# Kernel optimization log

Hardware: AMD Instinct MI355X
Metric: run time of the kernel (lower is better)

## Reference

```python
import jax, jax.numpy as jnp
import numpy as np
import math

B, T, D, H = 4, 2048, 1024, 16
DH = D // H

def setup_inputs() -> dict:
    key = jax.random.key(0)
    ks = jax.random.split(key, 5)
    scale = 1.0 / math.sqrt(D)
    x = jax.random.normal(ks[0], (B, T, D), dtype=jnp.float32)
    Wq = jax.random.normal(ks[1], (D, D), dtype=jnp.float32) * scale
    Wk = jax.random.normal(ks[2], (D, D), dtype=jnp.float32) * scale
    Wv = jax.random.normal(ks[3], (D, D), dtype=jnp.float32) * scale
    Wo = jax.random.normal(ks[4], (D, D), dtype=jnp.float32) * scale
    mask = jnp.tril(jnp.ones((T, T), dtype=jnp.int32))  # causal, 1=keep
    return {"x": x, "mask": mask, "Wq": Wq, "Wk": Wk, "Wv": Wv, "Wo": Wo}

def reference(x, mask, Wq, Wk, Wv, Wo):
    Bx, Tx, Dx = x.shape
    # nn.Linear(bias=False): y = x @ W.T
    q = (x @ Wq.T).reshape(Bx, Tx, H, DH).transpose(0, 2, 1, 3)  # [B,H,T,dh]
    k = (x @ Wk.T).reshape(Bx, Tx, H, DH).transpose(0, 2, 1, 3)
    v = (x @ Wv.T).reshape(Bx, Tx, H, DH).transpose(0, 2, 1, 3)
    scores = jnp.einsum('bhqd,bhkd->bhqk', q, k) / math.sqrt(DH)
    m = mask[None, None, :, :]  # [1,1,T,T]
    scores = scores + (m == 0).astype(scores.dtype) * -1e9
    attn = jax.nn.softmax(scores, axis=-1)  # stable (max-subtract) like original
    out = jnp.einsum('bhqk,bhkd->bhqd', attn, v)
    out = out.transpose(0, 2, 1, 3).reshape(Bx, Tx, Dx)
    return out @ Wo.T
```

## Files before the change

### kernel.cpp

```cpp
#include <hip/hip_runtime.h>
#include <stdint.h>

#define B_  4
#define T_  2048
#define D_  1024
#define H_  16
#define DH_ 64

typedef unsigned short u16;
typedef __attribute__((ext_vector_type(8))) short bf16x8;
typedef __attribute__((ext_vector_type(8))) unsigned short u16x8;
typedef __attribute__((ext_vector_type(4))) unsigned short u16x4;
typedef __attribute__((ext_vector_type(4))) float f32x4;

#define NT_ ((size_t)B_ * T_ * D_)
#define QSCALE 0.18033688011112043f

__device__ __forceinline__ u16 f2bf(float f) {
    union { float f; uint32_t u; } v; v.f = f;
    uint32_t r = v.u + 0x7FFFu + ((v.u >> 16) & 1u);
    return (u16)(r >> 16);
}

__device__ __forceinline__ uint32_t pack2(float lo, float hi) {
    union { float f; uint32_t u; } a, b; a.f = lo; b.f = hi;
    return __builtin_amdgcn_perm(b.u, a.u, 0x07060302u);
}

__device__ __forceinline__ void gl2lds16(const u16* g, u16* l) {
    __builtin_amdgcn_global_load_lds(
        (const __attribute__((address_space(1))) unsigned int*)g,
        (__attribute__((address_space(3))) unsigned int*)l,
        16, 0, 0);
}

#define VMCNT(n) asm volatile("s_waitcnt vmcnt(" #n ")" ::: "memory")

__global__ __launch_bounds__(256) void cvt_x_kernel(
    const float* __restrict__ src, u16* __restrict__ dst, int n8)
{
    int i = blockIdx.x * 256 + threadIdx.x;
    if (i >= n8) return;
    f32x4 a = ((const f32x4*)src)[2 * i];
    f32x4 b = ((const f32x4*)src)[2 * i + 1];
    u16x8 o;
    o[0]=f2bf(a[0]); o[1]=f2bf(a[1]); o[2]=f2bf(a[2]); o[3]=f2bf(a[3]);
    o[4]=f2bf(b[0]); o[5]=f2bf(b[1]); o[6]=f2bf(b[2]); o[7]=f2bf(b[3]);
    ((u16x8*)dst)[i] = o;
}

__global__ __launch_bounds__(256) void cvt_w_kernel(
    const float* __restrict__ w0, const float* __restrict__ w1,
    const float* __restrict__ w2, const float* __restrict__ w3,
    u16* __restrict__ dst)
{
    const float* src = (blockIdx.y == 0) ? w0 : (blockIdx.y == 1) ? w1
                     : (blockIdx.y == 2) ? w2 : w3;
    u16* d = dst + (size_t)blockIdx.y * (D_ * D_);
    int i = blockIdx.x * 256 + threadIdx.x;
    f32x4 a = ((const f32x4*)src)[2 * i];
    f32x4 b = ((const f32x4*)src)[2 * i + 1];
    u16x8 o;
    o[0]=f2bf(a[0]); o[1]=f2bf(a[1]); o[2]=f2bf(a[2]); o[3]=f2bf(a[3]);
    o[4]=f2bf(b[0]); o[5]=f2bf(b[1]); o[6]=f2bf(b[2]); o[7]=f2bf(b[3]);
    ((u16x8*)d)[i] = o;
}

template<int OUT_MODE>
__global__ __launch_bounds__(512) void gemm8_kernel(
    const u16* __restrict__ X, const u16* __restrict__ W,
    void* __restrict__ C, int M, int N, int K)
{
    __shared__ __align__(16) u16 Ab2[2][256 * 64];
    __shared__ __align__(16) u16 Bb2[2][256 * 64];

    const int tid  = threadIdx.x;
    const int wave = tid >> 6;
    const int lane = tid & 63;
    const int lq = lane >> 4, lm = lane & 15;
    const int wm = wave >> 2;
    const int wn = wave & 3;

    const int GX  = M >> 8;
    const int nwg = GX * (N >> 8);
    const int cpx = nwg >> 3;
    const int swz = ((int)blockIdx.x & 7) * cpx + ((int)blockIdx.x >> 3);
    const int m0 = (swz % GX) << 8;
    const int n0 = (swz / GX) << 8;

    const int srow = wave * 8 + (lane >> 3);
    const int scol = ((lane & 7) ^ (lane >> 3)) << 3;
    const u16* gA = X + (size_t)(m0 + srow) * K + scol;
    const u16* gB = W + (size_t)(n0 + srow) * K + scol;
    const size_t rK64 = (size_t)64 * K;

    const int swzr = (lm & 7) << 4;

    f32x4 acc[8][4] = {};
    const int NT = K >> 6;

    gl2lds16(gA,            Ab2[0] + wave * 512);
    gl2lds16(gA + rK64,     Ab2[0] + 4096  + wave * 512);
    gl2lds16(gA + 2 * rK64, Ab2[0] + 8192  + wave * 512);
    gl2lds16(gA + 3 * rK64, Ab2[0] + 12288 + wave * 512);
    gl2lds16(gB,            Bb2[0] + wave * 512);
    gl2lds16(gB + rK64,     Bb2[0] + 4096  + wave * 512);
    gl2lds16(gB + 2 * rK64, Bb2[0] + 8192  + wave * 512);
    gl2lds16(gB + 3 * rK64, Bb2[0] + 12288 + wave * 512);
    gl2lds16(gB + 64,            Bb2[1] + wave * 512);
    gl2lds16(gB + 64 + rK64,     Bb2[1] + 4096  + wave * 512);
    gl2lds16(gB + 64 + 2 * rK64, Bb2[1] + 8192  + wave * 512);
    gl2lds16(gB + 64 + 3 * rK64, Bb2[1] + 12288 + wave * 512);
    VMCNT(4);
    __builtin_amdgcn_s_barrier();

#pragma unroll 1
    for (int t = 0; t < NT; ++t) {
        const u16* Ablds = Ab2[t & 1];
        const u16* Bblds = Bb2[t & 1];
        u16* Abn = Ab2[(t & 1) ^ 1];
        u16* Bbc = Bb2[t & 1];
        const bool stA = (t + 1 < NT);
        const bool stB = (t + 2 < NT);
        const u16* gAs = gA + (size_t)(t + 1) * 64;
        const u16* gBs = gB + (size_t)(t + 2) * 64;
        bf16x8 bq[4][2];
#pragma unroll
        for (int q = 0; q < 4; ++q) {
            bf16x8 af[2][2];
#pragma unroll
            for (int i2 = 0; i2 < 2; ++i2)
#pragma unroll
                for (int ks = 0; ks < 2; ++ks) {
                    int off = (wm * 128 + (2 * q + i2) * 16 + lm) * 128
                            + ks * 64 + lq * 16;
                    af[i2][ks] = *(const bf16x8*)((const char*)Ablds + (off ^ swzr));
                }
            if (q == 0) {
#pragma unroll
                for (int j = 0; j < 4; ++j)
#pragma unroll
                    for (int ks = 0; ks < 2; ++ks) {
                        int off = (wn * 64 + j * 16 + lm) * 128
                                + ks * 64 + lq * 16;
                        bq[j][ks] = *(const bf16x8*)((const char*)Bblds + (off ^ swzr));
                    }
                if (stA) {
                    gl2lds16(gAs,        Abn + wave * 512);
                    gl2lds16(gAs + rK64, Abn + 4096 + wave * 512);
                }
            }
            if (q == 1 && stA) {
                gl2lds16(gAs + 2 * rK64, Abn + 8192  + wave * 512);
                gl2lds16(gAs + 3 * rK64, Abn + 12288 + wave * 512);
            }
            if (q == 2 && stB) {
                gl2lds16(gBs,        Bbc + wave * 512);
                gl2lds16(gBs + rK64, Bbc + 4096 + wave * 512);
            }
            if (q == 3 && stB) {
                gl2lds16(gBs + 2 * rK64, Bbc + 8192  + wave * 512);
                gl2lds16(gBs + 3 * rK64, Bbc + 12288 + wave * 512);
            }
            __builtin_amdgcn_s_barrier();
            asm volatile("s_waitcnt lgkmcnt(0)" ::: "memory");
            __builtin_amdgcn_sched_barrier(0);
            __builtin_amdgcn_s_setprio(1);
#pragma unroll
            for (int ks = 0; ks < 2; ++ks)
#pragma unroll
                for (int i2 = 0; i2 < 2; ++i2)
#pragma unroll
                    for (int j = 0; j < 4; ++j)
                        acc[2 * q + i2][j] = __builtin_amdgcn_mfma_f32_16x16x32_bf16(
                            af[i2][ks], bq[j][ks], acc[2 * q + i2][j], 0, 0, 0);
            __builtin_amdgcn_s_setprio(0);
            if (q == 3) {
                if (stB)      { VMCNT(4); }
                else if (stA) { VMCNT(0); }
            }
            __builtin_amdgcn_s_barrier();
        }
    }

    const int region = n0 >> 10;
#pragma unroll
    for (int i = 0; i < 8; ++i)
#pragma unroll
        for (int j = 0; j < 4; ++j) {
            int rowb = m0 + wm * 128 + i * 16 + lq * 4;
            int col  = n0 + wn * 64 + j * 16 + lm;
            if (OUT_MODE == 2) {
#pragma unroll
                for (int r = 0; r < 4; ++r)
                    ((float*)C)[(size_t)(rowb + r) * N + col] = acc[i][j][r];
            } else {
                u16* Qp = (u16*)C;
                int colr = col & 1023;
                if (region == 0) {
#pragma unroll
                    for (int r = 0; r < 4; ++r)
                        Qp[(size_t)(rowb + r) * D_ + colr] = f2bf(acc[i][j][r] * QSCALE);
                } else if (region == 1) {
#pragma unroll
                    for (int r = 0; r < 4; ++r)
                        (Qp + NT_)[(size_t)(rowb + r) * D_ + colr] = f2bf(acc[i][j][r]);
                } else {
                    int b = rowb >> 11, tt = rowb & (T_ - 1);
                    u16x4 pk;
#pragma unroll
                    for (int r = 0; r < 4; ++r) pk[r] = f2bf(acc[i][j][r]);
                    *(u16x4*)((Qp + 2 * NT_) + ((size_t)b * D_ + colr) * T_ + tt) = pk;
                }
            }
        }
}

__global__ __launch_bounds__(128) void attn_kernel(
    const u16* __restrict__ Qg, const u16* __restrict__ Kg,
    const u16* __restrict__ Vtg, u16* __restrict__ Og)
{
    __shared__ __align__(16) u16 Pl[2 * 64 * 40];
    __shared__ __align__(16) float Oc[16 * 64 * 4];
    __shared__ __align__(16) float Lc[4 * 64];

    const int tid  = threadIdx.x;
    const int wave = tid >> 6;
    const int lane = tid & 63;
    const int lq = lane >> 4, lm = lane & 15;
    const int id = blockIdx.x;
    const int xs = id & 7;
    const int k8 = id >> 3;
    const int bh = xs + 8 * (k8 & 7);
    const int pi = k8 >> 3;
    const int b = bh >> 4, h = bh & 15;

    const size_t batchoff = (size_t)b * T_ * D_;
    const size_t headoff  = (size_t)h * DH_;
    const size_t vbase    = (size_t)bh * DH_ * T_;

    u16* pw = Pl + wave * 64 * 40;

#pragma unroll 1
    for (int ph = 0; ph < 2; ++ph) {
        const int qj  = ph ? (31 - pi) : pi;
        const int qw  = qj * 64;
        const int ktd = qj >> 1;
        const int odd = qj & 1;

        bf16x8 aq[4][2];
#pragma unroll
        for (int qf = 0; qf < 4; ++qf) {
            const u16* qrow = Qg + batchoff + (size_t)(qw + qf * 16 + lm) * D_ + headoff;
            aq[qf][0] = *(const bf16x8*)(qrow + lq * 8);
            aq[qf][1] = *(const bf16x8*)(qrow + 32 + lq * 8);
        }

        f32x4 oaccT[4][4] = {};
        float l_lane[4] = {0.f, 0.f, 0.f, 0.f};

#pragma unroll 1
        for (int kt = wave; kt <= ktd; kt += 2) {
            const bool diag = (kt == ktd);
            const int ksmax = diag ? (odd ? 3 : 1) : 3;

#pragma unroll
            for (int c = 0; c < 4; ++c) {
                if (c <= ksmax) {
#pragma unroll
                    for (int t = 0; t < 2; ++t) {
                        const int mt = 2 * c + t;
                        const u16* krow = Kg + batchoff
                            + (size_t)(kt * 128 + mt * 16 + lm) * D_ + headoff;
                        bf16x8 kf0 = *(const bf16x8*)(krow + lq * 8);
                        bf16x8 kf1 = *(const bf16x8*)(krow + 32 + lq * 8);
                        f32x4 s[4];
#pragma unroll
                        for (int qf = 0; qf < 4; ++qf) {
                            s[qf] = f32x4{0.f, 0.f, 0.f, 0.f};
                            s[qf] = __builtin_amdgcn_mfma_f32_16x16x32_bf16(
                                kf0, aq[qf][0], s[qf], 0, 0, 0);
                            s[qf] = __builtin_amdgcn_mfma_f32_16x16x32_bf16(
                                kf1, aq[qf][1], s[qf], 0, 0, 0);
                        }
                        if (diag) {
                            int keyb = kt * 128 + mt * 16 + lq * 4;
#pragma unroll
                            for (int qf = 0; qf < 4; ++qf) {
                                int query = qw + qf * 16 + lm;
#pragma unroll
                                for (int r = 0; r < 4; ++r)
                                    if (keyb + r > query) s[qf][r] = -1e9f;
                            }
                        }
#pragma unroll
                        for (int qf = 0; qf < 4; ++qf) {
                            float p0 = __builtin_amdgcn_exp2f(s[qf][0]);
                            float p1 = __builtin_amdgcn_exp2f(s[qf][1]);
                            float p2 = __builtin_amdgcn_exp2f(s[qf][2]);
                            float p3 = __builtin_amdgcn_exp2f(s[qf][3]);
                            l_lane[qf] += (p0 + p1) + (p2 + p3);
                            uint2 d; d.x = pack2(p0, p1); d.y = pack2(p2, p3);
                            *(uint2*)(pw + (qf * 16 + lm) * 40 + t * 16 + lq * 4) = d;
                        }
                    }

                    bf16x8 pf[4];
#pragma unroll
                    for (int qf = 0; qf < 4; ++qf)
                        pf[qf] = *(const bf16x8*)(pw + (qf * 16 + lm) * 40 + lq * 8);
#pragma unroll
                    for (int mo = 0; mo < 4; ++mo) {
                        const u16* vrow = Vtg + vbase
                            + (size_t)(mo * 16 + lm) * T_ + kt * 128 + c * 32;
                        bf16x8 vf = *(const bf16x8*)(vrow + lq * 8);
#pragma unroll
                        for (int qf = 0; qf < 4; ++qf)
                            oaccT[qf][mo] = __builtin_amdgcn_mfma_f32_16x16x32_bf16(
                                vf, pf[qf], oaccT[qf][mo], 0, 0, 0);
                    }
                }
            }
        }

        if (wave == 1) {
#pragma unroll
            for (int qf = 0; qf < 4; ++qf) {
#pragma unroll
                for (int mo = 0; mo < 4; ++mo)
                    *(f32x4*)&Oc[((qf * 4 + mo) * 64 + lane) * 4] = oaccT[qf][mo];
                Lc[qf * 64 + lane] = l_lane[qf];
            }
        }
        __syncthreads();
        if (wave == 0) {
#pragma unroll
            for (int qf = 0; qf < 4; ++qf) {
#pragma unroll
                for (int mo = 0; mo < 4; ++mo) {
                    f32x4 o = *(const f32x4*)&Oc[((qf * 4 + mo) * 64 + lane) * 4];
#pragma unroll
                    for (int r = 0; r < 4; ++r) oaccT[qf][mo][r] += o[r];
                }
                l_lane[qf] += Lc[qf * 64 + lane];
            }
#pragma unroll
            for (int qf = 0; qf < 4; ++qf) {
                float l = l_lane[qf];
                l += __shfl_xor(l, 16, 64);
                l += __shfl_xor(l, 32, 64);
                float inv = 1.0f / l;
                int row = qw + qf * 16 + lm;
                u16* obase = Og + batchoff + (size_t)row * D_ + headoff;
#pragma unroll
                for (int mo = 0; mo < 4; ++mo) {
                    uint2 d;
                    d.x = pack2(oaccT[qf][mo][0] * inv, oaccT[qf][mo][1] * inv);
                    d.y = pack2(oaccT[qf][mo][2] * inv, oaccT[qf][mo][3] * inv);
                    *(uint2*)(obase + mo * 16 + lq * 4) = d;
                }
            }
        }
        __syncthreads();
    }
}

extern "C" void kernel_launch(void* const* d_in, const int* in_sizes, int n_in,
                              void* d_out, int out_size, void* d_ws, size_t ws_size,
                              hipStream_t stream)
{
    const float* x  = (const float*)d_in[0];
    const float* Wq = (const float*)d_in[2];
    const float* Wk = (const float*)d_in[3];
    const float* Wv = (const float*)d_in[4];
    const float* Wo = (const float*)d_in[5];

    const size_t DD = (size_t)D_ * D_;
    u16* Qb  = (u16*)d_ws;
    u16* Kb  = Qb + NT_;
    u16* Vb  = Kb + NT_;
    u16* Ob  = Vb + NT_;
    u16* xb  = Ob + NT_;
    u16* wb  = xb + NT_;

    const int M = B_ * T_;

    cvt_x_kernel<<<dim3((int)(NT_ / 8 / 256)), 256, 0, stream>>>(x, xb, (int)(NT_ / 8));
    cvt_w_kernel<<<dim3((int)(DD / 8 / 256), 4), 256, 0, stream>>>(Wq, Wk, Wv, Wo, wb);

    gemm8_kernel<3><<<dim3((M / 256) * (3 * D_ / 256)), 512, 0, stream>>>(
        xb, wb, Qb, M, 3 * D_, D_);

    attn_kernel<<<dim3(1024), 128, 0, stream>>>(Qb, Kb, Vb, Ob);

    gemm8_kernel<2><<<dim3((M / 256) * (D_ / 256)), 512, 0, stream>>>(
        Ob, wb + 3 * DD, d_out, M, D_, D_);
}
```

Baseline: 287.9 us.

## Prefetch next-tile B fragments, remap XCD tiles, use 128-tile output GEMM

The 256x256 GEMM now prefetches half of the next K-tile's B fragments from LDS during the last two quarter-steps and carries them in registers. This hides LDS read latency at the start of each tile, at the cost of extra registers and reworked vmcnt waits. The workgroup-to-tile mapping is changed so each XCD owns a contiguous 2D block of M and N tiles, intended to improve L2 reuse. The output projection switches to a new simple 128x128, 256-thread GEMM that is single-buffered with no LDS swizzle, giving more workgroups for the smaller N=1024 problem.

After: 290.0 us. Within noise of the previous version (+0.7%).

```diff
diff --git a/kernel.cpp b/kernel.cpp
--- a/kernel.cpp
+++ b/kernel.cpp
@@ -35,6 +35,12 @@
 }
 
 #define VMCNT(n) asm volatile("s_waitcnt vmcnt(" #n ")" ::: "memory")
+
+__device__ __forceinline__ bf16x8 ldsrd(const u16* base, int row, int ks,
+                                        int lq, int swzr) {
+    int off = row * 128 + ks * 64 + lq * 16;
+    return *(const bf16x8*)((const char*)base + (off ^ swzr));
+}
 
 __global__ __launch_bounds__(256) void cvt_x_kernel(
     const float* __restrict__ src, u16* __restrict__ dst, int n8)
@@ -82,11 +88,12 @@
     const int wn = wave & 3;
 
     const int GX  = M >> 8;
-    const int nwg = GX * (N >> 8);
-    const int cpx = nwg >> 3;
-    const int swz = ((int)blockIdx.x & 7) * cpx + ((int)blockIdx.x >> 3);
-    const int m0 = (swz % GX) << 8;
-    const int n0 = (swz / GX) << 8;
+    const int rm  = GX >> 2;
+    const int rn  = (N >> 8) >> 1;
+    const int xcd = (int)blockIdx.x & 7;
+    const int idx = (int)blockIdx.x >> 3;
+    const int m0 = ((xcd & 3) * rm + (idx % rm)) << 8;
+    const int n0 = ((xcd >> 2) * rn + (idx / rm)) << 8;
 
     const int srow = wave * 8 + (lane >> 3);
     const int scol = ((lane & 7) ^ (lane >> 3)) << 3;
@@ -97,6 +104,7 @@
     const int swzr = (lm & 7) << 4;
 
     f32x4 acc[8][4] = {};
+    bf16x8 bq01[2][2], bq23[2][2], bqn01[2][2];
     const int NT = K >> 6;
 
     gl2lds16(gA,            Ab2[0] + wave * 512);
@@ -113,38 +121,40 @@
     gl2lds16(gB + 64 + 3 * rK64, Bb2[1] + 12288 + wave * 512);
     VMCNT(4);
     __builtin_amdgcn_s_barrier();
+#pragma unroll
+    for (int j = 0; j < 2; ++j)
+#pragma unroll
+        for (int ks = 0; ks < 2; ++ks)
+            bq01[j][ks] = ldsrd(Bb2[0], wn * 64 + j * 16 + lm, ks, lq, swzr);
 
 #pragma unroll 1
     for (int t = 0; t < NT; ++t) {
         const u16* Ablds = Ab2[t & 1];
         const u16* Bblds = Bb2[t & 1];
+        const u16* Bbn   = Bb2[(t & 1) ^ 1];
         u16* Abn = Ab2[(t & 1) ^ 1];
         u16* Bbc = Bb2[t & 1];
         const bool stA = (t + 1 < NT);
         const bool stB = (t + 2 < NT);
+        const bool pfB = (t + 1 < NT);
         const u16* gAs = gA + (size_t)(t + 1) * 64;
         const u16* gBs = gB + (size_t)(t + 2) * 64;
-        bf16x8 bq[4][2];
 #pragma unroll
         for (int q = 0; q < 4; ++q) {
             bf16x8 af[2][2];
 #pragma unroll
             for (int i2 = 0; i2 < 2; ++i2)
 #pragma unroll
-                for (int ks = 0; ks < 2; ++ks) {
-                    int off = (wm * 128 + (2 * q + i2) * 16 + lm) * 128
-                            + ks * 64 + lq * 16;
-                    af[i2][ks] = *(const bf16x8*)((const char*)Ablds + (off ^ swzr));
-                }
+                for (int ks = 0; ks < 2; ++ks)
+                    af[i2][ks] = ldsrd(Ablds,
+                        wm * 128 + (2 * q + i2) * 16 + lm, ks, lq, swzr);
             if (q == 0) {
 #pragma unroll
-                for (int j = 0; j < 4; ++j)
-#pragma unroll
-                    for (int ks = 0; ks < 2; ++ks) {
-                        int off = (wn * 64 + j * 16 + lm) * 128
-                                + ks * 64 + lq * 16;
-                        bq[j][ks] = *(const bf16x8*)((const char*)Bblds + (off ^ swzr));
-                    }
+                for (int j2 = 0; j2 < 2; ++j2)
+#pragma unroll
+                    for (int ks = 0; ks < 2; ++ks)
+                        bq23[j2][ks] = ldsrd(Bblds,
+                            wn * 64 + (2 + j2) * 16 + lm, ks, lq, swzr);
                 if (stA) {
                     gl2lds16(gAs,        Abn + wave * 512);
                     gl2lds16(gAs + rK64, Abn + 4096 + wave * 512);
@@ -154,13 +164,27 @@
                 gl2lds16(gAs + 2 * rK64, Abn + 8192  + wave * 512);
                 gl2lds16(gAs + 3 * rK64, Abn + 12288 + wave * 512);
             }
-            if (q == 2 && stB) {
-                gl2lds16(gBs,        Bbc + wave * 512);
-                gl2lds16(gBs + rK64, Bbc + 4096 + wave * 512);
-            }
-            if (q == 3 && stB) {
-                gl2lds16(gBs + 2 * rK64, Bbc + 8192  + wave * 512);
-                gl2lds16(gBs + 3 * rK64, Bbc + 12288 + wave * 512);
+            if (q == 2) {
+                if (pfB) {
+#pragma unroll
+                    for (int ks = 0; ks < 2; ++ks)
+                        bqn01[0][ks] = ldsrd(Bbn, wn * 64 + lm, ks, lq, swzr);
+                }
+                if (stB) {
+                    gl2lds16(gBs,        Bbc + wave * 512);
+                    gl2lds16(gBs + rK64, Bbc + 4096 + wave * 512);
+                }
+            }
+            if (q == 3) {
+                if (pfB) {
+#pragma unroll
+                    for (int ks = 0; ks < 2; ++ks)
+                        bqn01[1][ks] = ldsrd(Bbn, wn * 64 + 16 + lm, ks, lq, swzr);
+                }
+                if (stB) {
+                    gl2lds16(gBs + 2 * rK64, Bbc + 8192  + wave * 512);
+                    gl2lds16(gBs + 3 * rK64, Bbc + 12288 + wave * 512);
+                }
             }
             __builtin_amdgcn_s_barrier();
             asm volatile("s_waitcnt lgkmcnt(0)" ::: "memory");
@@ -169,17 +193,32 @@
 #pragma unroll
             for (int ks = 0; ks < 2; ++ks)
 #pragma unroll
-                for (int i2 = 0; i2 < 2; ++i2)
-#pragma unroll
-                    for (int j = 0; j < 4; ++j)
-                        acc[2 * q + i2][j] = __builtin_amdgcn_mfma_f32_16x16x32_bf16(
-                            af[i2][ks], bq[j][ks], acc[2 * q + i2][j], 0, 0, 0);
+                for (int i2 = 0; i2 < 2; ++i2) {
+                    acc[2 * q + i2][0] = __builtin_amdgcn_mfma_f32_16x16x32_bf16(
+                        af[i2][ks], bq01[0][ks], acc[2 * q + i2][0], 0, 0, 0);
+                    acc[2 * q + i2][1] = __builtin_amdgcn_mfma_f32_16x16x32_bf16(
+                        af[i2][ks], bq01[1][ks], acc[2 * q + i2][1], 0, 0, 0);
+                    acc[2 * q + i2][2] = __builtin_amdgcn_mfma_f32_16x16x32_bf16(
+                        af[i2][ks], bq23[0][ks], acc[2 * q + i2][2], 0, 0, 0);
+                    acc[2 * q + i2][3] = __builtin_amdgcn_mfma_f32_16x16x32_bf16(
+                        af[i2][ks], bq23[1][ks], acc[2 * q + i2][3], 0, 0, 0);
+                }
             __builtin_amdgcn_s_setprio(0);
+            if (q == 1) {
+                if (t < NT - 1) { VMCNT(4); }
+            }
             if (q == 3) {
-                if (stB)      { VMCNT(4); }
-                else if (stA) { VMCNT(0); }
+                if (t < NT - 2)       { VMCNT(4); }
+                else if (t == NT - 2) { VMCNT(0); }
             }
             __builtin_amdgcn_s_barrier();
+        }
+        if (t + 1 < NT) {
+#pragma unroll
+            for (int j = 0; j < 2; ++j)
+#pragma unroll
+                for (int ks = 0; ks < 2; ++ks)
+                    bq01[j][ks] = bqn01[j][ks];
         }
     }
 
@@ -213,6 +252,70 @@
                     *(u16x4*)((Qp + 2 * NT_) + ((size_t)b * D_ + colr) * T_ + tt) = pk;
                 }
             }
+        }
+}
+
+__global__ __launch_bounds__(256) void gemm_bt_kernel(
+    const u16* __restrict__ X, const u16* __restrict__ W,
+    float* __restrict__ C, int M, int N, int K)
+{
+    __shared__ __align__(16) u16 As[128 * 64];
+    __shared__ __align__(16) u16 Bs[128 * 64];
+
+    const int tid  = threadIdx.x;
+    const int wave = tid >> 6;
+    const int lane = tid & 63;
+    const int lq = lane >> 4;
+    const int lm = lane & 15;
+    const int m0 = blockIdx.x * 128;
+    const int n0 = blockIdx.y * 128;
+    const int wm = (wave & 1) * 64;
+    const int wn = (wave >> 1) * 64;
+
+    f32x4 acc[4][4] = {};
+
+    const int r0 = wave * 32 + (lane >> 3);
+    const int c0 = (lane & 7) * 8;
+    const u16* gA = X + (size_t)(m0 + r0) * K + c0;
+    const u16* gB = W + (size_t)(n0 + r0) * K + c0;
+    u16* lA = As + wave * 32 * 64;
+    u16* lB = Bs + wave * 32 * 64;
+
+    for (int k0 = 0; k0 < K; k0 += 64) {
+#pragma unroll
+        for (int p = 0; p < 4; ++p) {
+            gl2lds16(gA + (size_t)p * 8 * K + k0, lA + p * 8 * 64);
+            gl2lds16(gB + (size_t)p * 8 * K + k0, lB + p * 8 * 64);
+        }
+        __syncthreads();
+#pragma unroll
+        for (int ks = 0; ks < 2; ++ks) {
+            bf16x8 af[4], bfr[4];
+#pragma unroll
+            for (int t = 0; t < 4; ++t)
+                af[t] = *(const bf16x8*)(As + (wm + t * 16 + lm) * 64 + ks * 32 + lq * 8);
+#pragma unroll
+            for (int t = 0; t < 4; ++t)
+                bfr[t] = *(const bf16x8*)(Bs + (wn + t * 16 + lm) * 64 + ks * 32 + lq * 8);
+#pragma unroll
+            for (int i = 0; i < 4; ++i)
+#pragma unroll
+                for (int j = 0; j < 4; ++j)
+                    acc[i][j] = __builtin_amdgcn_mfma_f32_16x16x32_bf16(
+                        af[i], bfr[j], acc[i][j], 0, 0, 0);
+        }
+        __syncthreads();
+    }
+
+#pragma unroll
+    for (int i = 0; i < 4; ++i)
+#pragma unroll
+        for (int j = 0; j < 4; ++j) {
+            int rowb = m0 + wm + i * 16 + lq * 4;
+            int col  = n0 + wn + j * 16 + lm;
+#pragma unroll
+            for (int r = 0; r < 4; ++r)
+                C[(size_t)(rowb + r) * N + col] = acc[i][j][r];
         }
 }
 
@@ -393,6 +496,6 @@
 
     attn_kernel<<<dim3(1024), 128, 0, stream>>>(Qb, Kb, Vb, Ob);
 
-    gemm8_kernel<2><<<dim3((M / 256) * (D_ / 256)), 512, 0, stream>>>(
-        Ob, wb + 3 * DD, d_out, M, D_, D_);
-}
+    gemm_bt_kernel<<<dim3(M / 128, D_ / 128), 256, 0, stream>>>(
+        Ob, wb + 3 * DD, (float*)d_out, M, D_, D_);
+}
```
